# Performance work log

Measured on AMD Instinct MI355X. Metric: run time of the kernel, lower is better.

Reference implementation:

```python
import jax, jax.numpy as jnp
import numpy as np


def setup_inputs() -> dict:
    key = jax.random.key(0)
    k1, k2, k3, k4, k5 = jax.random.split(key, 5)
    num_chunks, input_dim, output_dim = 100000, 256, 512
    num_members, num_cells = 400000, 50000
    chunk_features = jax.random.normal(k1, (num_chunks, input_dim), dtype=jnp.float32)
    member_idx = jax.random.randint(k2, (num_members,), 0, num_chunks, dtype=jnp.int32)
    segment_ids = jnp.sort(jax.random.randint(k3, (num_members,), 0, num_cells, dtype=jnp.int32))
    W = jax.random.normal(k4, (input_dim, output_dim), dtype=jnp.float32) / np.sqrt(input_dim)
    b = jax.random.normal(k5, (output_dim,), dtype=jnp.float32) * 0.01
    return {
        "chunk_features": chunk_features,
        "member_idx": member_idx,
        "segment_ids": segment_ids,
        "num_cells": num_cells,
        "W": W,
        "b": b,
    }


def reference(chunk_features, member_idx, segment_ids, num_cells, W, b):
    # Gather per-membership chunk embeddings: (M, D)
    gathered = jnp.take(chunk_features, member_idx, axis=0)
    # Segment-sum over cells, then divide by counts -> segment mean (num_cells, D)
    sums = jax.ops.segment_sum(gathered, segment_ids, num_segments=num_cells)
    counts = jax.ops.segment_sum(
        jnp.ones((member_idx.shape[0],), dtype=chunk_features.dtype),
        segment_ids, num_segments=num_cells)
    cell_emb = sums / jnp.maximum(counts, 1.0)[:, None]
    # Linear projection (input_dim != output_dim)
    return cell_emb @ W + b
```

## Files before the change

kernel.cpp:

```cpp
#include <hip/hip_runtime.h>

typedef __attribute__((ext_vector_type(8))) short short8;
typedef __attribute__((ext_vector_type(8))) unsigned short ushort8;
typedef __attribute__((ext_vector_type(4))) float floatx4;

static __device__ __forceinline__ unsigned short f2bf(float f) {
    unsigned int u = __float_as_uint(f);
    u = (u + 0x7FFFu + ((u >> 16) & 1u)) >> 16;
    return (unsigned short)u;
}
static __device__ __forceinline__ float bf2f(unsigned short h) {
    return __uint_as_float(((unsigned int)h) << 16);
}

__global__ __launch_bounds__(256) void prep_kernel(
        const float* __restrict__ cf, int cast_elems,
        const int* __restrict__ seg, int M, int num_cells,
        const float* __restrict__ W,
        unsigned short* __restrict__ cf16,
        int* __restrict__ starts,
        unsigned short* __restrict__ Wt,
        int castB, int startB) {
    const int b = blockIdx.x;
    const int tid = threadIdx.x;
    if (b < castB) {
        int g = (b * 256 + tid) * 8;
        if (g + 8 <= cast_elems) {
            float4 a = *(const float4*)(cf + g);
            float4 c = *(const float4*)(cf + g + 4);
            short8 o;
            o[0] = (short)f2bf(a.x); o[1] = (short)f2bf(a.y);
            o[2] = (short)f2bf(a.z); o[3] = (short)f2bf(a.w);
            o[4] = (short)f2bf(c.x); o[5] = (short)f2bf(c.y);
            o[6] = (short)f2bf(c.z); o[7] = (short)f2bf(c.w);
            *(short8*)(cf16 + g) = o;
        } else {
            for (int i = g; i < cast_elems; ++i) cf16[i] = f2bf(cf[i]);
        }
    } else if (b < castB + startB) {
        int m = (b - castB) * 256 + tid;
        if (m > M) return;
        int prev = (m == 0) ? -1 : seg[m - 1];
        int cur  = (m == M) ? num_cells : seg[m];
        for (int c = prev + 1; c <= cur; ++c) starts[c] = m;
    } else {
        int g = (b - castB - startB) * 256 + tid;
        if (g < 512 * 256) {
            int n = g >> 8, k = g & 255;
            Wt[g] = f2bf(W[k * 512 + n]);
        }
    }
}

__global__ __launch_bounds__(256) void seg_mean_kernel(
        const unsigned short* __restrict__ cf16,
        const int* __restrict__ member_idx,
        const int* __restrict__ starts,
        int num_cells,
        unsigned short* __restrict__ cell_emb) {
    const int wid  = threadIdx.x >> 6;
    const int lane = threadIdx.x & 63;
    const int half = lane >> 5;
    const int li   = lane & 31;
    const int c = blockIdx.x * 4 + wid;

    float acc[8] = {0.f, 0.f, 0.f, 0.f, 0.f, 0.f, 0.f, 0.f};
    int cnt = 0;

    if (c < num_cells) {
        const int s = starts[c];
        const int e = starts[c + 1];
        cnt = e - s;

        for (int base = s; base < e; base += 64) {
            int m = base + lane;
            int idx = (m < e) ? member_idx[m] : 0;
            int n = e - base; if (n > 64) n = 64;
            int npairs2 = n & ~1;
            for (int j0 = 0; j0 < npairs2; j0 += 16) {
                ushort8 v[8];
#pragma unroll
                for (int p = 0; p < 8; ++p) {
                    int jj = j0 + 2 * p;
                    if (jj < npairs2) {
                        int ciA = __shfl(idx, jj);
                        int ciB = __shfl(idx, jj + 1);
                        int ci  = half ? ciB : ciA;
                        v[p] = *(const ushort8*)(cf16 + (size_t)ci * 256 + li * 8);
                    }
                }
#pragma unroll
                for (int p = 0; p < 8; ++p) {
                    int jj = j0 + 2 * p;
                    if (jj < npairs2) {
#pragma unroll
                        for (int t = 0; t < 8; ++t) acc[t] += bf2f(v[p][t]);
                    }
                }
            }
            if (n & 1) {
                int ci = __shfl(idx, n - 1);
                if (!half) {
                    ushort8 v = *(const ushort8*)(cf16 + (size_t)ci * 256 + li * 8);
#pragma unroll
                    for (int t = 0; t < 8; ++t) acc[t] += bf2f(v[t]);
                }
            }
        }
    }

    float inv = (cnt > 0) ? 1.0f / (float)cnt : 0.f;
    if (c < num_cells && cnt == 0) inv = 0.f;
#pragma unroll
    for (int t = 0; t < 8; ++t)
        acc[t] += __shfl_xor(acc[t], 32);
    if (!half) {
        ushort8 o;
#pragma unroll
        for (int t = 0; t < 8; ++t) o[t] = f2bf(acc[t] * inv);
        *(ushort8*)(cell_emb + (size_t)c * 256 + li * 8) = o;
    }
}

__global__ __launch_bounds__(256) void gemm_kernel(
        const unsigned short* __restrict__ A,
        const unsigned short* __restrict__ Bt,
        const float* __restrict__ bias,
        float* __restrict__ out,
        int Mreal) {
    constexpr int LDSS = 40;
    __shared__ unsigned short As[128 * LDSS];
    __shared__ unsigned short Bs[128 * LDSS];

    const int tid  = threadIdx.x;
    const int wid  = tid >> 6;
    const int lane = tid & 63;
    const int wm = wid & 1, wn = wid >> 1;
    const int l15 = lane & 15, q = lane >> 4;
    const int m0 = blockIdx.y * 128;
    const int n0 = blockIdx.x * 128;

    floatx4 acc[4][4] = {};

    for (int kb = 0; kb < 256; kb += 32) {
#pragma unroll
        for (int r = 0; r < 2; ++r) {
            int chunk = tid + r * 256;
            int row = chunk >> 2;
            int col = (chunk & 3) * 8;
            *(short8*)&As[row * LDSS + col] =
                *(const short8*)&A[(size_t)(m0 + row) * 256 + kb + col];
            *(short8*)&Bs[row * LDSS + col] =
                *(const short8*)&Bt[(size_t)(n0 + row) * 256 + kb + col];
        }
        __syncthreads();

        short8 af[4], bf[4];
#pragma unroll
        for (int mi = 0; mi < 4; ++mi)
            af[mi] = *(const short8*)&As[(wm * 64 + mi * 16 + l15) * LDSS + q * 8];
#pragma unroll
        for (int ni = 0; ni < 4; ++ni)
            bf[ni] = *(const short8*)&Bs[(wn * 64 + ni * 16 + l15) * LDSS + q * 8];
#pragma unroll
        for (int mi = 0; mi < 4; ++mi)
#pragma unroll
            for (int ni = 0; ni < 4; ++ni)
                acc[mi][ni] = __builtin_amdgcn_mfma_f32_16x16x32_bf16(
                    af[mi], bf[ni], acc[mi][ni], 0, 0, 0);
        __syncthreads();
    }

#pragma unroll
    for (int ni = 0; ni < 4; ++ni) {
        int n = n0 + wn * 64 + ni * 16 + l15;
        float bv = bias[n];
#pragma unroll
        for (int mi = 0; mi < 4; ++mi) {
            int mbase = m0 + wm * 64 + mi * 16 + q * 4;
#pragma unroll
            for (int r = 0; r < 4; ++r) {
                int row = mbase + r;
                if (row < Mreal)
                    out[(size_t)row * 512 + n] = acc[mi][ni][r] + bv;
            }
        }
    }
}

extern "C" void kernel_launch(void* const* d_in, const int* in_sizes, int n_in,
                              void* d_out, int out_size, void* d_ws, size_t ws_size,
                              hipStream_t stream) {
    const float* chunk_features = (const float*)d_in[0];
    const int*   member_idx     = (const int*)d_in[1];
    const int*   segment_ids    = (const int*)d_in[2];
    const float* W              = (const float*)d_in[4];
    const float* bias           = (const float*)d_in[5];
    float* out = (float*)d_out;

    const int cast_elems = in_sizes[0];
    const int M          = in_sizes[1];
    const int out_dim    = in_sizes[5];
    const int num_cells  = out_size / out_dim;
    const int mtiles = (num_cells + 127) / 128;
    const int Mpad   = mtiles * 128;

    unsigned short* cell_emb = (unsigned short*)d_ws;
    unsigned short* Wt       = cell_emb + (size_t)Mpad * 256;
    unsigned short* cf16     = Wt + 512 * 256;
    int*            starts   = (int*)(cf16 + (((size_t)cast_elems + 7) & ~7ull));

    const int castB  = (cast_elems + 2047) / 2048;
    const int startB = (M + 1 + 255) / 256;
    const int wtB    = (512 * 256 + 255) / 256;

    hipLaunchKernelGGL(prep_kernel, dim3(castB + startB + wtB), dim3(256), 0, stream,
                       chunk_features, cast_elems, segment_ids, M, num_cells, W,
                       cf16, starts, Wt, castB, startB);
    hipLaunchKernelGGL(seg_mean_kernel, dim3(Mpad / 4), dim3(256), 0, stream,
                       cf16, member_idx, starts, num_cells, cell_emb);
    hipLaunchKernelGGL(gemm_kernel, dim3(4, mtiles), dim3(256), 0, stream,
                       cell_emb, Wt, bias, out, num_cells);
}
```

Measured before the change: 273.9 us.

## Gather fp32 features directly and drop the bf16 cast pass over the chunk table

Removes the prep-stage conversion of the whole chunk feature table to bf16. The segment-mean kernel now gathers fp32 rows directly, with each lane loading a float4 and a whole wavefront covering one row, instead of two half-waves each reading a bf16 row. This saves a full read-and-write pass over the table, but each gathered row is now twice as large. Whether it pays off depends on how well the roughly 100MB fp32 table stays resident in the large last-level cache during the random gathers.

```diff
diff --git a/kernel.cpp b/kernel.cpp
--- a/kernel.cpp
+++ b/kernel.cpp
@@ -1,7 +1,7 @@
 #include <hip/hip_runtime.h>
 
 typedef __attribute__((ext_vector_type(8))) short short8;
-typedef __attribute__((ext_vector_type(8))) unsigned short ushort8;
+typedef __attribute__((ext_vector_type(4))) unsigned short ushort4v;
 typedef __attribute__((ext_vector_type(4))) float floatx4;
 
 static __device__ __forceinline__ unsigned short f2bf(float f) {
@@ -9,42 +9,23 @@
     u = (u + 0x7FFFu + ((u >> 16) & 1u)) >> 16;
     return (unsigned short)u;
 }
-static __device__ __forceinline__ float bf2f(unsigned short h) {
-    return __uint_as_float(((unsigned int)h) << 16);
-}
 
 __global__ __launch_bounds__(256) void prep_kernel(
-        const float* __restrict__ cf, int cast_elems,
         const int* __restrict__ seg, int M, int num_cells,
         const float* __restrict__ W,
-        unsigned short* __restrict__ cf16,
         int* __restrict__ starts,
         unsigned short* __restrict__ Wt,
-        int castB, int startB) {
+        int startB) {
     const int b = blockIdx.x;
     const int tid = threadIdx.x;
-    if (b < castB) {
-        int g = (b * 256 + tid) * 8;
-        if (g + 8 <= cast_elems) {
-            float4 a = *(const float4*)(cf + g);
-            float4 c = *(const float4*)(cf + g + 4);
-            short8 o;
-            o[0] = (short)f2bf(a.x); o[1] = (short)f2bf(a.y);
-            o[2] = (short)f2bf(a.z); o[3] = (short)f2bf(a.w);
-            o[4] = (short)f2bf(c.x); o[5] = (short)f2bf(c.y);
-            o[6] = (short)f2bf(c.z); o[7] = (short)f2bf(c.w);
-            *(short8*)(cf16 + g) = o;
-        } else {
-            for (int i = g; i < cast_elems; ++i) cf16[i] = f2bf(cf[i]);
-        }
-    } else if (b < castB + startB) {
-        int m = (b - castB) * 256 + tid;
+    if (b < startB) {
+        int m = b * 256 + tid;
         if (m > M) return;
         int prev = (m == 0) ? -1 : seg[m - 1];
         int cur  = (m == M) ? num_cells : seg[m];
         for (int c = prev + 1; c <= cur; ++c) starts[c] = m;
     } else {
-        int g = (b - castB - startB) * 256 + tid;
+        int g = (b - startB) * 256 + tid;
         if (g < 512 * 256) {
             int n = g >> 8, k = g & 255;
             Wt[g] = f2bf(W[k * 512 + n]);
@@ -53,18 +34,16 @@
 }
 
 __global__ __launch_bounds__(256) void seg_mean_kernel(
-        const unsigned short* __restrict__ cf16,
+        const float* __restrict__ cf,
         const int* __restrict__ member_idx,
         const int* __restrict__ starts,
         int num_cells,
         unsigned short* __restrict__ cell_emb) {
     const int wid  = threadIdx.x >> 6;
     const int lane = threadIdx.x & 63;
-    const int half = lane >> 5;
-    const int li   = lane & 31;
     const int c = blockIdx.x * 4 + wid;
 
-    float acc[8] = {0.f, 0.f, 0.f, 0.f, 0.f, 0.f, 0.f, 0.f};
+    float acc[4] = {0.f, 0.f, 0.f, 0.f};
     int cnt = 0;
 
     if (c < num_cells) {
@@ -76,50 +55,33 @@
             int m = base + lane;
             int idx = (m < e) ? member_idx[m] : 0;
             int n = e - base; if (n > 64) n = 64;
-            int npairs2 = n & ~1;
-            for (int j0 = 0; j0 < npairs2; j0 += 16) {
-                ushort8 v[8];
+            for (int j0 = 0; j0 < n; j0 += 8) {
+                float4 v[8];
 #pragma unroll
                 for (int p = 0; p < 8; ++p) {
-                    int jj = j0 + 2 * p;
-                    if (jj < npairs2) {
-                        int ciA = __shfl(idx, jj);
-                        int ciB = __shfl(idx, jj + 1);
-                        int ci  = half ? ciB : ciA;
-                        v[p] = *(const ushort8*)(cf16 + (size_t)ci * 256 + li * 8);
+                    int j = j0 + p;
+                    if (j < n) {
+                        int ci = __shfl(idx, j);
+                        v[p] = *(const float4*)(cf + (size_t)ci * 256 + lane * 4);
                     }
                 }
 #pragma unroll
                 for (int p = 0; p < 8; ++p) {
-                    int jj = j0 + 2 * p;
-                    if (jj < npairs2) {
-#pragma unroll
-                        for (int t = 0; t < 8; ++t) acc[t] += bf2f(v[p][t]);
+                    int j = j0 + p;
+                    if (j < n) {
+                        acc[0] += v[p].x; acc[1] += v[p].y;
+                        acc[2] += v[p].z; acc[3] += v[p].w;
                     }
-                }
-            }
-            if (n & 1) {
-                int ci = __shfl(idx, n - 1);
-                if (!half) {
-                    ushort8 v = *(const ushort8*)(cf16 + (size_t)ci * 256 + li * 8);
-#pragma unroll
-                    for (int t = 0; t < 8; ++t) acc[t] += bf2f(v[t]);
                 }
             }
         }
     }
 
     float inv = (cnt > 0) ? 1.0f / (float)cnt : 0.f;
-    if (c < num_cells && cnt == 0) inv = 0.f;
+    ushort4v o;
 #pragma unroll
-    for (int t = 0; t < 8; ++t)
-        acc[t] += __shfl_xor(acc[t], 32);
-    if (!half) {
-        ushort8 o;
-#pragma unroll
-        for (int t = 0; t < 8; ++t) o[t] = f2bf(acc[t] * inv);
-        *(ushort8*)(cell_emb + (size_t)c * 256 + li * 8) = o;
-    }
+    for (int t = 0; t < 4; ++t) o[t] = f2bf(acc[t] * inv);
+    *(ushort4v*)(cell_emb + (size_t)c * 256 + lane * 4) = o;
 }
 
 __global__ __launch_bounds__(256) void gemm_kernel(
@@ -198,7 +160,6 @@
     const float* bias           = (const float*)d_in[5];
     float* out = (float*)d_out;
 
-    const int cast_elems = in_sizes[0];
     const int M          = in_sizes[1];
     const int out_dim    = in_sizes[5];
     const int num_cells  = out_size / out_dim;
@@ -207,18 +168,15 @@
 
     unsigned short* cell_emb = (unsigned short*)d_ws;
     unsigned short* Wt       = cell_emb + (size_t)Mpad * 256;
-    unsigned short* cf16     = Wt + 512 * 256;
-    int*            starts   = (int*)(cf16 + (((size_t)cast_elems + 7) & ~7ull));
+    int*            starts   = (int*)(Wt + 512 * 256);
 
-    const int castB  = (cast_elems + 2047) / 2048;
     const int startB = (M + 1 + 255) / 256;
     const int wtB    = (512 * 256 + 255) / 256;
 
-    hipLaunchKernelGGL(prep_kernel, dim3(castB + startB + wtB), dim3(256), 0, stream,
-                       chunk_features, cast_elems, segment_ids, M, num_cells, W,
-                       cf16, starts, Wt, castB, startB);
+    hipLaunchKernelGGL(prep_kernel, dim3(startB + wtB), dim3(256), 0, stream,
+                       segment_ids, M, num_cells, W, starts, Wt, startB);
     hipLaunchKernelGGL(seg_mean_kernel, dim3(Mpad / 4), dim3(256), 0, stream,
-                       cf16, member_idx, starts, num_cells, cell_emb);
+                       chunk_features, member_idx, starts, num_cells, cell_emb);
     hipLaunchKernelGGL(gemm_kernel, dim3(4, mtiles), dim3(256), 0, stream,
                        cell_emb, Wt, bias, out, num_cells);
 }
```

Measured after the change: 278.6 us, median of 3. About the same (+1.7%).
